# Performance work log

Hardware: AMD Instinct MI355X
Metric: run time of the kernel (lower is better)

Reference implementation:

```python
import jax, jax.numpy as jnp
import numpy as np

N = 50000        # nodes
E = 800000       # edges (before self-loops)
IN = 128         # in_dim
HID = 32         # hidden_dim per head
HEADS = 4
OUT = 64         # out_dim
NEG_SLOPE = 0.2  # PyG GATConv default leaky_relu slope


def setup_inputs() -> dict:
    key = jax.random.key(0)
    ks = jax.random.split(key, 10)
    g = lambda k, shape: jax.random.normal(k, shape, jnp.float32) * 0.1
    x = jax.random.normal(ks[0], (N, IN), jnp.float32)
    edge_index = jax.random.randint(ks[1], (2, E), 0, N, dtype=jnp.int64)
    W1 = g(ks[2], (IN, HEADS * HID))
    att_src1 = g(ks[3], (HEADS, HID))
    att_dst1 = g(ks[4], (HEADS, HID))
    b1 = jnp.zeros((HEADS * HID,), jnp.float32)
    W2 = g(ks[5], (HEADS * HID, OUT))
    att_src2 = g(ks[6], (1, OUT))
    att_dst2 = g(ks[7], (1, OUT))
    b2 = jnp.zeros((OUT,), jnp.float32)
    return {"x": x, "edge_index": edge_index,
            "W1": W1, "att_src1": att_src1, "att_dst1": att_dst1, "b1": b1,
            "W2": W2, "att_src2": att_src2, "att_dst2": att_dst2, "b2": b2}


def gat_layer(x, src, dst, W, a_src, a_dst, b, concat):
    """One PyG-style GATConv layer (self-loops already in src/dst)."""
    H, C = a_src.shape
    h = (x @ W).reshape(-1, H, C)                       # [N, H, C]
    al_s = jnp.sum(h * a_src, axis=-1)                  # [N, H]
    al_d = jnp.sum(h * a_dst, axis=-1)                  # [N, H]
    e = jax.nn.leaky_relu(al_s[src] + al_d[dst], NEG_SLOPE)  # [E', H]
    # segment softmax over incoming edges of each destination node
    m = jax.ops.segment_max(e, dst, num_segments=N)
    m = jnp.where(jnp.isfinite(m), m, 0.0)
    ex = jnp.exp(e - m[dst])
    denom = jax.ops.segment_sum(ex, dst, num_segments=N)
    alpha = ex / (denom[dst] + 1e-16)                   # [E', H]
    out = jax.ops.segment_sum(alpha[:, :, None] * h[src], dst, num_segments=N)  # [N,H,C]
    out = out.reshape(-1, H * C) if concat else out.mean(axis=1)
    return out + b


def reference(x, edge_index, W1, att_src1, att_dst1, b1, W2, att_src2, att_dst2, b2):
    src, dst = edge_index[0], edge_index[1]
    loop = jnp.arange(N, dtype=src.dtype)               # add_self_loops=True default
    src = jnp.concatenate([src, loop])
    dst = jnp.concatenate([dst, loop])
    h = gat_layer(x, src, dst, W1, att_src1, att_dst1, b1, concat=True)   # [N, HEADS*HID]
    h = jax.nn.elu(h)
    return gat_layer(h, src, dst, W2, att_src2, att_dst2, b2, concat=False)  # [N, OUT]
```

## Files before the change

kernel.cpp:

```cpp
#include <hip/hip_runtime.h>

#define NN 50000
#define EE 800000
#define NB 196
#define CHUNK 2048
#define NBLK ((EE + CHUNK - 1) / CHUNK)
#define CAP 6144
#define SSTR 6400

typedef unsigned int uint;
typedef unsigned short ushort;
typedef __attribute__((ext_vector_type(8))) short bf16x8;
typedef __attribute__((ext_vector_type(4))) float f32x4;

__device__ __forceinline__ float lrelu(float v){ return v > 0.f ? v : 0.2f*v; }
__device__ __forceinline__ ushort bf16r(float a){
  uint ua = __float_as_uint(a);
  return (ushort)((ua + 0x7FFFu + ((ua >> 16) & 1u)) >> 16);
}
__device__ __forceinline__ uint pack_bf16(float a, float b){
  return (uint)bf16r(a) | ((uint)bf16r(b) << 16);
}
__device__ __forceinline__ float bf_lo(uint u){ return __uint_as_float(u << 16); }
__device__ __forceinline__ float bf_hi(uint u){ return __uint_as_float(u & 0xFFFF0000u); }

__global__ __launch_bounds__(256) void k_zero(int* __restrict__ ecur){
  int t = threadIdx.x;
  if (t < NB) ecur[t] = 0;
}

__global__ __launch_bounds__(256) void k_bucketize(const int* __restrict__ ei,
                                                   int* __restrict__ ecur, uint* __restrict__ ebuf){
  __shared__ int h[NB];
  __shared__ int sc[256];
  __shared__ int gdelta[NB];
  __shared__ uint P[CHUNK];
  __shared__ int  A[CHUNK];
  int t = threadIdx.x;
  if (t < NB) h[t] = 0;
  __syncthreads();
  int base = blockIdx.x * CHUNK;
  int end = base + CHUNK; if (end > EE) end = EE;
  int bc = end - base;
  int be[8]; int re[8]; uint pe[8];
  #pragma unroll
  for (int q = 0; q < 8; ++q){
    int i = base + t + q*256;
    be[q] = -1;
    if (i < end){
      int s_ = ei[i], d_ = ei[EE + i];
      pe[q] = ((uint)d_ << 16) | (uint)s_;
      int bb = d_ >> 8;
      be[q] = bb;
      re[q] = atomicAdd(&h[bb], 1);
    }
  }
  __syncthreads();
  int v = (t < NB) ? h[t] : 0;
  sc[t] = v;
  __syncthreads();
  for (int off = 1; off < 256; off <<= 1){
    int add = (t >= off) ? sc[t-off] : 0;
    __syncthreads();
    sc[t] += add;
    __syncthreads();
  }
  if (t < NB){
    int lofs = sc[t] - v;
    int g = v ? atomicAdd(&ecur[t], v) : 0;
    gdelta[t] = t*CAP + g - lofs;
    h[t] = lofs;
  }
  __syncthreads();
  #pragma unroll
  for (int q = 0; q < 8; ++q) if (be[q] >= 0){
    int j = h[be[q]] + re[q];
    P[j] = pe[q];
    A[j] = gdelta[be[q]] + j;
  }
  __syncthreads();
  for (int j = t; j < bc; j += 256) ebuf[A[j]] = P[j];
}

__global__ __launch_bounds__(256) void k_csr(const int* __restrict__ ecur,
                                             const uint* __restrict__ ebuf,
                                             int* __restrict__ rptr, int* __restrict__ rend,
                                             ushort* __restrict__ csr){
  __shared__ uint  sbuf[CAP];
  __shared__ ushort rnk[CAP];
  __shared__ int h[256];
  __shared__ int sc[256];
  int b = blockIdx.x, t = threadIdx.x;
  int nd0 = b * 256;
  int ncnt = NN - nd0; if (ncnt > 256) ncnt = 256;
  int cnt = ecur[b]; if (cnt > CAP) cnt = CAP;
  int e0 = b * CAP;
  int cb = b * SSTR;
  h[t] = (t < ncnt) ? 1 : 0;
  for (int j = t; j < cnt; j += 256) sbuf[j] = ebuf[e0 + j];
  __syncthreads();
  for (int j = t; j < cnt; j += 256){
    int local = (sbuf[j] >> 16) & 255;
    rnk[j] = (ushort)atomicAdd(&h[local], 1);
  }
  __syncthreads();
  int v = h[t];
  sc[t] = v;
  __syncthreads();
  for (int off = 1; off < 256; off <<= 1){
    int add = (t >= off) ? sc[t-off] : 0;
    __syncthreads();
    sc[t] += add;
    __syncthreads();
  }
  h[t] = sc[t] - v;
  __syncthreads();
  if (t < ncnt){
    int rs = cb + h[t];
    rptr[nd0 + t] = rs;
    rend[nd0 + t] = rs + v;
    csr[rs] = (ushort)(nd0 + t);
  }
  for (int j = t; j < cnt; j += 256){
    uint p = sbuf[j];
    int local = (p >> 16) & 255;
    csr[cb + h[local] + (int)rnk[j]] = (ushort)(p & 0xFFFFu);
  }
}

__global__ __launch_bounds__(256, 3) void k_gemm1(const float* __restrict__ x, const float* __restrict__ W,
    const float* __restrict__ a_src, const float* __restrict__ a_dst,
    uint* __restrict__ h1b, float* __restrict__ al_s, float* __restrict__ al_d){
  __shared__ ushort Wt[128*136];
  __shared__ ushort Ash[64*136];
  int tid = threadIdx.x;
  int row0 = blockIdx.x * 64;
  const float4* W4 = (const float4*)W;
  #pragma unroll
  for (int f0 = 0; f0 < 4096; f0 += 256){
    int idx4 = f0 + tid;
    int k = idx4 >> 5;
    int n0 = (idx4 & 31) * 4;
    float4 v = W4[idx4];
    Wt[(n0  )*136 + k] = bf16r(v.x);
    Wt[(n0+1)*136 + k] = bf16r(v.y);
    Wt[(n0+2)*136 + k] = bf16r(v.z);
    Wt[(n0+3)*136 + k] = bf16r(v.w);
  }
  const float4* x4 = (const float4*)x;
  #pragma unroll
  for (int f0 = 0; f0 < 2048; f0 += 256){
    int idx4 = f0 + tid;
    int row = idx4 >> 5;
    int q = idx4 & 31;
    float4 v = make_float4(0.f,0.f,0.f,0.f);
    if (row0 + row < NN) v = x4[(size_t)(row0+row)*32 + q];
    *(uint2*)(Ash + row*136 + q*4) = make_uint2(pack_bf16(v.x, v.y), pack_bf16(v.z, v.w));
  }
  __syncthreads();

  int w = tid >> 6, lane = tid & 63;
  int lm = lane & 15, lg = lane >> 4;
  const ushort* Ab = Ash + (w*16 + lm)*136 + lg*8;
  const ushort* Bb = Wt + lm*136 + lg*8;
  f32x4 acc[8];
  #pragma unroll
  for (int i = 0; i < 8; ++i) acc[i] = (f32x4){0.f,0.f,0.f,0.f};
  #pragma unroll
  for (int ks = 0; ks < 4; ++ks){
    bf16x8 af = *(const bf16x8*)(Ab + ks*32);
    #pragma unroll
    for (int ct = 0; ct < 8; ++ct){
      bf16x8 bfr = *(const bf16x8*)(Bb + ct*16*136 + ks*32);
      acc[ct] = __builtin_amdgcn_mfma_f32_16x16x32_bf16(af, bfr, acc[ct], 0, 0, 0);
    }
  }
  int nbase = row0 + w*16 + lg*4;
  float ps[4][4], pd[4][4];
  #pragma unroll
  for (int h = 0; h < 4; ++h)
    #pragma unroll
    for (int r = 0; r < 4; ++r){ ps[h][r] = 0.f; pd[h][r] = 0.f; }
  #pragma unroll
  for (int ct = 0; ct < 8; ++ct){
    int col = ct*16 + lm;
    float ac = a_src[col], dc = a_dst[col];
    #pragma unroll
    for (int r = 0; r < 4; ++r){
      float v = acc[ct][r];
      ps[ct>>1][r] += v*ac;
      pd[ct>>1][r] += v*dc;
      float vp = __shfl_xor(v, 1);
      if ((lm & 1) == 0 && nbase + r < NN)
        h1b[(size_t)(nbase+r)*64 + ct*8 + (lm>>1)] = pack_bf16(v, vp);
    }
  }
  #pragma unroll
  for (int h = 0; h < 4; ++h)
    #pragma unroll
    for (int r = 0; r < 4; ++r){
      float s = ps[h][r], d = pd[h][r];
      s += __shfl_xor(s,1); s += __shfl_xor(s,2); s += __shfl_xor(s,4); s += __shfl_xor(s,8);
      d += __shfl_xor(d,1); d += __shfl_xor(d,2); d += __shfl_xor(d,4); d += __shfl_xor(d,8);
      if (lm == 0 && nbase + r < NN){
        al_s[(nbase+r)*4 + h] = s;
        al_d[(nbase+r)*4 + h] = d;
      }
    }
}

__global__ __launch_bounds__(256) void k_agg1(const int* __restrict__ rptr, const int* __restrict__ rend,
    const ushort* __restrict__ csr,
    const uint* __restrict__ h1b, const float* __restrict__ al_s, const float* __restrict__ al_d,
    const float* __restrict__ b1, uint* __restrict__ h2b){
  int wid  = (blockIdx.x*256 + threadIdx.x) >> 6;
  int lane = threadIdx.x & 63;
  if (wid >= NN) return;
  int half = lane >> 5;
  int li   = lane & 31;
  int h    = li >> 3;
  float ad = al_d[(uint)(wid*4 + h)];
  int rs = rptr[wid];
  int deg = rend[wid] - rs;
  uint rowoff = (uint)(li*2);
  float a0 = 0.f, a1 = 0.f, a2 = 0.f, a3 = 0.f, den = 0.f;
  for (int b0 = 0; b0 < deg; b0 += 64){
    int nb = deg - b0; if (nb > 64) nb = 64;
    int sv = (lane < nb) ? (int)csr[(uint)(rs + b0 + lane)] : 0;
    int jj = 0;
    for (; jj + 8 <= nb; jj += 8){
      int j = jj + half;
      int s0 = __shfl(sv, j), s1 = __shfl(sv, j+2), s2 = __shfl(sv, j+4), s3 = __shfl(sv, j+6);
      float e0 = al_s[(uint)(s0*4 + h)];
      float e1 = al_s[(uint)(s1*4 + h)];
      float e2 = al_s[(uint)(s2*4 + h)];
      float e3 = al_s[(uint)(s3*4 + h)];
      uint2 u0 = *(const uint2*)(h1b + (((uint)s0) << 6) + rowoff);
      uint2 u1 = *(const uint2*)(h1b + (((uint)s1) << 6) + rowoff);
      uint2 u2 = *(const uint2*)(h1b + (((uint)s2) << 6) + rowoff);
      uint2 u3 = *(const uint2*)(h1b + (((uint)s3) << 6) + rowoff);
      float x0 = __expf(lrelu(e0 + ad));
      float x1 = __expf(lrelu(e1 + ad));
      float x2 = __expf(lrelu(e2 + ad));
      float x3 = __expf(lrelu(e3 + ad));
      den += x0 + x1 + x2 + x3;
      a0 += x0*bf_lo(u0.x) + x1*bf_lo(u1.x) + x2*bf_lo(u2.x) + x3*bf_lo(u3.x);
      a1 += x0*bf_hi(u0.x) + x1*bf_hi(u1.x) + x2*bf_hi(u2.x) + x3*bf_hi(u3.x);
      a2 += x0*bf_lo(u0.y) + x1*bf_lo(u1.y) + x2*bf_lo(u2.y) + x3*bf_lo(u3.y);
      a3 += x0*bf_hi(u0.y) + x1*bf_hi(u1.y) + x2*bf_hi(u2.y) + x3*bf_hi(u3.y);
    }
    for (; jj < nb; jj += 2){
      int j = jj + half;
      bool ok = j < nb;
      int s0 = __shfl(sv, ok ? j : 0);
      float e = al_s[(uint)(s0*4 + h)];
      uint2 u = *(const uint2*)(h1b + (((uint)s0) << 6) + rowoff);
      float ex = ok ? __expf(lrelu(e + ad)) : 0.f;
      den += ex;
      a0 += ex*bf_lo(u.x); a1 += ex*bf_hi(u.x);
      a2 += ex*bf_lo(u.y); a3 += ex*bf_hi(u.y);
    }
  }
  den += __shfl_xor(den, 32);
  a0  += __shfl_xor(a0, 32);
  a1  += __shfl_xor(a1, 32);
  a2  += __shfl_xor(a2, 32);
  a3  += __shfl_xor(a3, 32);
  if (half == 0){
    float inv = 1.f/(den + 1e-16f);
    float4 bb = *(const float4*)(b1 + li*4);
    float o0 = a0*inv + bb.x, o1 = a1*inv + bb.y, o2 = a2*inv + bb.z, o3 = a3*inv + bb.w;
    o0 = o0 > 0.f ? o0 : (__expf(o0) - 1.f);
    o1 = o1 > 0.f ? o1 : (__expf(o1) - 1.f);
    o2 = o2 > 0.f ? o2 : (__expf(o2) - 1.f);
    o3 = o3 > 0.f ? o3 : (__expf(o3) - 1.f);
    *(uint2*)(h2b + (size_t)wid*64 + li*2) = make_uint2(pack_bf16(o0,o1), pack_bf16(o2,o3));
  }
}

__global__ __launch_bounds__(256, 4) void k_gemm2(const uint* __restrict__ h2b, const float* __restrict__ W,
    const float* __restrict__ a_src, const float* __restrict__ a_dst,
    uint* __restrict__ gb, float* __restrict__ al_s, float* __restrict__ al_d){
  __shared__ ushort Wt[64*136];
  __shared__ ushort Ash[64*136];
  int tid = threadIdx.x;
  int row0 = blockIdx.x * 64;
  const float4* W4 = (const float4*)W;
  #pragma unroll
  for (int f0 = 0; f0 < 2048; f0 += 256){
    int idx4 = f0 + tid;
    int k = idx4 >> 4;
    int n0 = (idx4 & 15) * 4;
    float4 v = W4[idx4];
    Wt[(n0  )*136 + k] = bf16r(v.x);
    Wt[(n0+1)*136 + k] = bf16r(v.y);
    Wt[(n0+2)*136 + k] = bf16r(v.z);
    Wt[(n0+3)*136 + k] = bf16r(v.w);
  }
  #pragma unroll
  for (int f0 = 0; f0 < 4096; f0 += 256){
    int idx = f0 + tid;
    int row = idx >> 6;
    int q = idx & 63;
    uint u = 0;
    if (row0 + row < NN) u = h2b[(size_t)(row0+row)*64 + q];
    *(uint*)(Ash + row*136 + q*2) = u;
  }
  __syncthreads();

  int w = tid >> 6, lane = tid & 63;
  int lm = lane & 15, lg = lane >> 4;
  const ushort* Ab = Ash + (w*16 + lm)*136 + lg*8;
  const ushort* Bb = Wt + lm*136 + lg*8;
  f32x4 acc[4];
  #pragma unroll
  for (int i = 0; i < 4; ++i) acc[i] = (f32x4){0.f,0.f,0.f,0.f};
  #pragma unroll
  for (int ks = 0; ks < 4; ++ks){
    bf16x8 af = *(const bf16x8*)(Ab + ks*32);
    #pragma unroll
    for (int ct = 0; ct < 4; ++ct){
      bf16x8 bfr = *(const bf16x8*)(Bb + ct*16*136 + ks*32);
      acc[ct] = __builtin_amdgcn_mfma_f32_16x16x32_bf16(af, bfr, acc[ct], 0, 0, 0);
    }
  }
  int nbase = row0 + w*16 + lg*4;
  float ps[4], pd[4];
  #pragma unroll
  for (int r = 0; r < 4; ++r){ ps[r] = 0.f; pd[r] = 0.f; }
  #pragma unroll
  for (int ct = 0; ct < 4; ++ct){
    int col = ct*16 + lm;
    float ac = a_src[col], dc = a_dst[col];
    #pragma unroll
    for (int r = 0; r < 4; ++r){
      float v = acc[ct][r];
      ps[r] += v*ac;
      pd[r] += v*dc;
      float vp = __shfl_xor(v, 1);
      if ((lm & 1) == 0 && nbase + r < NN)
        gb[(size_t)(nbase+r)*32 + ct*8 + (lm>>1)] = pack_bf16(v, vp);
    }
  }
  #pragma unroll
  for (int r = 0; r < 4; ++r){
    float s = ps[r], d = pd[r];
    s += __shfl_xor(s,1); s += __shfl_xor(s,2); s += __shfl_xor(s,4); s += __shfl_xor(s,8);
    d += __shfl_xor(d,1); d += __shfl_xor(d,2); d += __shfl_xor(d,4); d += __shfl_xor(d,8);
    if (lm == 0 && nbase + r < NN){
      al_s[nbase+r] = s;
      al_d[nbase+r] = d;
    }
  }
}

__global__ __launch_bounds__(256) void k_agg2(const int* __restrict__ rptr, const int* __restrict__ rend,
    const ushort* __restrict__ csr,
    const uint* __restrict__ gb, const float* __restrict__ al_s, const float* __restrict__ al_d,
    const float* __restrict__ b2, float* __restrict__ out){
  int wid  = (blockIdx.x*256 + threadIdx.x) >> 6;
  int lane = threadIdx.x & 63;
  if (wid >= NN) return;
  int half = lane >> 5;
  int li   = lane & 31;
  float ad = al_d[(uint)wid];
  int rs = rptr[wid];
  int deg = rend[wid] - rs;
  float a0 = 0.f, a1 = 0.f, den = 0.f;
  for (int b0 = 0; b0 < deg; b0 += 64){
    int nb = deg - b0; if (nb > 64) nb = 64;
    int sv = (lane < nb) ? (int)csr[(uint)(rs + b0 + lane)] : 0;
    int jj = 0;
    for (; jj + 8 <= nb; jj += 8){
      int j = jj + half;
      int s0 = __shfl(sv, j), s1 = __shfl(sv, j+2), s2 = __shfl(sv, j+4), s3 = __shfl(sv, j+6);
      float e0 = al_s[(uint)s0];
      float e1 = al_s[(uint)s1];
      float e2 = al_s[(uint)s2];
      float e3 = al_s[(uint)s3];
      uint u0 = gb[(((uint)s0) << 5) + (uint)li];
      uint u1 = gb[(((uint)s1) << 5) + (uint)li];
      uint u2 = gb[(((uint)s2) << 5) + (uint)li];
      uint u3 = gb[(((uint)s3) << 5) + (uint)li];
      float x0 = __expf(lrelu(e0 + ad));
      float x1 = __expf(lrelu(e1 + ad));
      float x2 = __expf(lrelu(e2 + ad));
      float x3 = __expf(lrelu(e3 + ad));
      den += x0 + x1 + x2 + x3;
      a0 += x0*bf_lo(u0) + x1*bf_lo(u1) + x2*bf_lo(u2) + x3*bf_lo(u3);
      a1 += x0*bf_hi(u0) + x1*bf_hi(u1) + x2*bf_hi(u2) + x3*bf_hi(u3);
    }
    for (; jj < nb; jj += 2){
      int j = jj + half;
      bool ok = j < nb;
      int s0 = __shfl(sv, ok ? j : 0);
      float e = al_s[(uint)s0];
      uint u = gb[(((uint)s0) << 5) + (uint)li];
      float ex = ok ? __expf(lrelu(e + ad)) : 0.f;
      den += ex;
      a0 += ex*bf_lo(u); a1 += ex*bf_hi(u);
    }
  }
  den += __shfl_xor(den, 32);
  a0  += __shfl_xor(a0, 32);
  a1  += __shfl_xor(a1, 32);
  if (half == 0){
    float inv = 1.f/(den + 1e-16f);
    float2 bb = *(const float2*)(b2 + li*2);
    *(float2*)(out + (size_t)wid*64 + li*2) = make_float2(a0*inv + bb.x, a1*inv + bb.y);
  }
}

extern "C" void kernel_launch(void* const* d_in, const int* in_sizes, int n_in,
                              void* d_out, int out_size, void* d_ws, size_t ws_size,
                              hipStream_t stream){
  const float* x   = (const float*)d_in[0];
  const int*   ei  = (const int*)d_in[1];
  const float* W1  = (const float*)d_in[2];
  const float* as1 = (const float*)d_in[3];
  const float* ad1 = (const float*)d_in[4];
  const float* b1  = (const float*)d_in[5];
  const float* W2  = (const float*)d_in[6];
  const float* as2 = (const float*)d_in[7];
  const float* ad2 = (const float*)d_in[8];
  const float* b2  = (const float*)d_in[9];
  float* out = (float*)d_out;
  (void)in_sizes; (void)n_in; (void)out_size; (void)ws_size;

  char* p = (char*)d_ws;
  size_t off = 0;
  auto alloc = [&](size_t bytes)->char*{
    char* r = p + off; off += (bytes + 255) & ~size_t(255); return r;
  };
  uint*  h1b   = (uint*)alloc((size_t)NN*64*4);
  uint*  h2b   = (uint*)alloc((size_t)NN*64*4);
  uint*  gb    = (uint*)alloc((size_t)NN*32*4);
  float* al1s  = (float*)alloc((size_t)NN*4*4);
  float* al1d  = (float*)alloc((size_t)NN*4*4);
  float* al2s  = (float*)alloc((size_t)NN*4);
  float* al2d  = (float*)alloc((size_t)NN*4);
  int*   rptr  = (int*)alloc((size_t)NN*4);
  int*   rend  = (int*)alloc((size_t)NN*4);
  ushort* csr  = (ushort*)alloc((size_t)NB*SSTR*2);
  uint*  ebuf  = (uint*)alloc((size_t)NB*CAP*4);
  int*   ecur  = (int*)alloc((size_t)NB*4);

  k_zero<<<1, 256, 0, stream>>>(ecur);
  k_bucketize<<<NBLK, 256, 0, stream>>>(ei, ecur, ebuf);
  k_csr<<<NB, 256, 0, stream>>>(ecur, ebuf, rptr, rend, csr);
  k_gemm1<<<(NN+63)/64, 256, 0, stream>>>(x, W1, as1, ad1, h1b, al1s, al1d);
  k_agg1<<<(NN*64+255)/256, 256, 0, stream>>>(rptr, rend, csr, h1b, al1s, al1d, b1, h2b);
  k_gemm2<<<(NN+63)/64, 256, 0, stream>>>(h2b, W2, as2, ad2, gb, al2s, al2d);
  k_agg2<<<(NN*64+255)/256, 256, 0, stream>>>(rptr, rend, csr, gb, al2s, al2d, b2, out);
}
```

Measured before the change: 137.1 us.

## Fuse bucketize with gemm1 and layer-1 aggregation with gemm2

Merges edge bucketizing and the layer-1 GEMM into one launch whose blocks split by block index, sharing shared memory through a union. Layer-1 aggregation is fused with the layer-2 GEMM: each 512-thread block aggregates 64 nodes into shared memory and then runs MFMA on them, which removes the h2b round trip through global memory. The zero kernel is replaced by a memset, and there are fewer launches overall. In exchange, the fused aggregation blocks are larger and heavier on registers and shared memory, which may lower occupancy and load balance for the gather phase.

```diff
diff --git a/kernel.cpp b/kernel.cpp
--- a/kernel.cpp
+++ b/kernel.cpp
@@ -5,6 +5,7 @@
 #define NB 196
 #define CHUNK 2048
 #define NBLK ((EE + CHUNK - 1) / CHUNK)
+#define GB1 ((NN + 63) / 64)
 #define CAP 6144
 #define SSTR 6400
 
@@ -24,62 +25,137 @@
 __device__ __forceinline__ float bf_lo(uint u){ return __uint_as_float(u << 16); }
 __device__ __forceinline__ float bf_hi(uint u){ return __uint_as_float(u & 0xFFFF0000u); }
 
-__global__ __launch_bounds__(256) void k_zero(int* __restrict__ ecur){
+union BG1Shared {
+  struct { int h[NB]; int sc[256]; int gdelta[NB]; uint P[CHUNK]; int A[CHUNK]; } bk;
+  struct { ushort Wt[128*136]; ushort Ash[64*136]; } gm;
+};
+
+__global__ __launch_bounds__(256, 3) void k_bg1(const int* __restrict__ ei,
+    int* __restrict__ ecur, uint* __restrict__ ebuf,
+    const float* __restrict__ x, const float* __restrict__ W,
+    const float* __restrict__ a_src, const float* __restrict__ a_dst,
+    uint* __restrict__ h1b, float* __restrict__ al_s, float* __restrict__ al_d){
+  __shared__ BG1Shared S;
   int t = threadIdx.x;
-  if (t < NB) ecur[t] = 0;
-}
-
-__global__ __launch_bounds__(256) void k_bucketize(const int* __restrict__ ei,
-                                                   int* __restrict__ ecur, uint* __restrict__ ebuf){
-  __shared__ int h[NB];
-  __shared__ int sc[256];
-  __shared__ int gdelta[NB];
-  __shared__ uint P[CHUNK];
-  __shared__ int  A[CHUNK];
-  int t = threadIdx.x;
-  if (t < NB) h[t] = 0;
-  __syncthreads();
-  int base = blockIdx.x * CHUNK;
-  int end = base + CHUNK; if (end > EE) end = EE;
-  int bc = end - base;
-  int be[8]; int re[8]; uint pe[8];
-  #pragma unroll
-  for (int q = 0; q < 8; ++q){
-    int i = base + t + q*256;
-    be[q] = -1;
-    if (i < end){
-      int s_ = ei[i], d_ = ei[EE + i];
-      pe[q] = ((uint)d_ << 16) | (uint)s_;
-      int bb = d_ >> 8;
-      be[q] = bb;
-      re[q] = atomicAdd(&h[bb], 1);
-    }
-  }
-  __syncthreads();
-  int v = (t < NB) ? h[t] : 0;
-  sc[t] = v;
-  __syncthreads();
-  for (int off = 1; off < 256; off <<= 1){
-    int add = (t >= off) ? sc[t-off] : 0;
-    __syncthreads();
-    sc[t] += add;
-    __syncthreads();
-  }
-  if (t < NB){
-    int lofs = sc[t] - v;
-    int g = v ? atomicAdd(&ecur[t], v) : 0;
-    gdelta[t] = t*CAP + g - lofs;
-    h[t] = lofs;
-  }
-  __syncthreads();
-  #pragma unroll
-  for (int q = 0; q < 8; ++q) if (be[q] >= 0){
-    int j = h[be[q]] + re[q];
-    P[j] = pe[q];
-    A[j] = gdelta[be[q]] + j;
-  }
-  __syncthreads();
-  for (int j = t; j < bc; j += 256) ebuf[A[j]] = P[j];
+  if (blockIdx.x < NBLK){
+    if (t < NB) S.bk.h[t] = 0;
+    __syncthreads();
+    int base = blockIdx.x * CHUNK;
+    int end = base + CHUNK; if (end > EE) end = EE;
+    int bc = end - base;
+    int be[8]; int re[8]; uint pe[8];
+    #pragma unroll
+    for (int q = 0; q < 8; ++q){
+      int i = base + t + q*256;
+      be[q] = -1;
+      if (i < end){
+        int s_ = ei[i], d_ = ei[EE + i];
+        pe[q] = ((uint)d_ << 16) | (uint)s_;
+        int bb = d_ >> 8;
+        be[q] = bb;
+        re[q] = atomicAdd(&S.bk.h[bb], 1);
+      }
+    }
+    __syncthreads();
+    int v = (t < NB) ? S.bk.h[t] : 0;
+    S.bk.sc[t] = v;
+    __syncthreads();
+    for (int off = 1; off < 256; off <<= 1){
+      int add = (t >= off) ? S.bk.sc[t-off] : 0;
+      __syncthreads();
+      S.bk.sc[t] += add;
+      __syncthreads();
+    }
+    if (t < NB){
+      int lofs = S.bk.sc[t] - v;
+      int g = v ? atomicAdd(&ecur[t], v) : 0;
+      S.bk.gdelta[t] = t*CAP + g - lofs;
+      S.bk.h[t] = lofs;
+    }
+    __syncthreads();
+    #pragma unroll
+    for (int q = 0; q < 8; ++q) if (be[q] >= 0){
+      int j = S.bk.h[be[q]] + re[q];
+      S.bk.P[j] = pe[q];
+      S.bk.A[j] = S.bk.gdelta[be[q]] + j;
+    }
+    __syncthreads();
+    for (int j = t; j < bc; j += 256) ebuf[S.bk.A[j]] = S.bk.P[j];
+    return;
+  }
+  int row0 = (blockIdx.x - NBLK) * 64;
+  const float4* W4 = (const float4*)W;
+  #pragma unroll
+  for (int f0 = 0; f0 < 4096; f0 += 256){
+    int idx4 = f0 + t;
+    int k = idx4 >> 5;
+    int n0 = (idx4 & 31) * 4;
+    float4 v = W4[idx4];
+    S.gm.Wt[(n0  )*136 + k] = bf16r(v.x);
+    S.gm.Wt[(n0+1)*136 + k] = bf16r(v.y);
+    S.gm.Wt[(n0+2)*136 + k] = bf16r(v.z);
+    S.gm.Wt[(n0+3)*136 + k] = bf16r(v.w);
+  }
+  const float4* x4 = (const float4*)x;
+  #pragma unroll
+  for (int f0 = 0; f0 < 2048; f0 += 256){
+    int idx4 = f0 + t;
+    int row = idx4 >> 5;
+    int q = idx4 & 31;
+    float4 v = make_float4(0.f,0.f,0.f,0.f);
+    if (row0 + row < NN) v = x4[(size_t)(row0+row)*32 + q];
+    *(uint2*)(S.gm.Ash + row*136 + q*4) = make_uint2(pack_bf16(v.x, v.y), pack_bf16(v.z, v.w));
+  }
+  __syncthreads();
+
+  int w = t >> 6, lane = t & 63;
+  int lm = lane & 15, lg = lane >> 4;
+  const ushort* Ab = S.gm.Ash + (w*16 + lm)*136 + lg*8;
+  const ushort* Bb = S.gm.Wt + lm*136 + lg*8;
+  f32x4 acc[8];
+  #pragma unroll
+  for (int i = 0; i < 8; ++i) acc[i] = (f32x4){0.f,0.f,0.f,0.f};
+  #pragma unroll
+  for (int ks = 0; ks < 4; ++ks){
+    bf16x8 af = *(const bf16x8*)(Ab + ks*32);
+    #pragma unroll
+    for (int ct = 0; ct < 8; ++ct){
+      bf16x8 bfr = *(const bf16x8*)(Bb + ct*16*136 + ks*32);
+      acc[ct] = __builtin_amdgcn_mfma_f32_16x16x32_bf16(af, bfr, acc[ct], 0, 0, 0);
+    }
+  }
+  int nbase = row0 + w*16 + lg*4;
+  float ps[4][4], pd[4][4];
+  #pragma unroll
+  for (int h = 0; h < 4; ++h)
+    #pragma unroll
+    for (int r = 0; r < 4; ++r){ ps[h][r] = 0.f; pd[h][r] = 0.f; }
+  #pragma unroll
+  for (int ct = 0; ct < 8; ++ct){
+    int col = ct*16 + lm;
+    float ac = a_src[col], dc = a_dst[col];
+    #pragma unroll
+    for (int r = 0; r < 4; ++r){
+      float v = acc[ct][r];
+      ps[ct>>1][r] += v*ac;
+      pd[ct>>1][r] += v*dc;
+      float vp = __shfl_xor(v, 1);
+      if ((lm & 1) == 0 && nbase + r < NN)
+        h1b[(size_t)(nbase+r)*64 + ct*8 + (lm>>1)] = pack_bf16(v, vp);
+    }
+  }
+  #pragma unroll
+  for (int h = 0; h < 4; ++h)
+    #pragma unroll
+    for (int r = 0; r < 4; ++r){
+      float s = ps[h][r], d = pd[h][r];
+      s += __shfl_xor(s,1); s += __shfl_xor(s,2); s += __shfl_xor(s,4); s += __shfl_xor(s,8);
+      d += __shfl_xor(d,1); d += __shfl_xor(d,2); d += __shfl_xor(d,4); d += __shfl_xor(d,8);
+      if (lm == 0 && nbase + r < NN){
+        al_s[(nbase+r)*4 + h] = s;
+        al_d[(nbase+r)*4 + h] = d;
+      }
+    }
 }
 
 __global__ __launch_bounds__(256) void k_csr(const int* __restrict__ ecur,
@@ -128,166 +204,21 @@
   }
 }
 
-__global__ __launch_bounds__(256, 3) void k_gemm1(const float* __restrict__ x, const float* __restrict__ W,
-    const float* __restrict__ a_src, const float* __restrict__ a_dst,
-    uint* __restrict__ h1b, float* __restrict__ al_s, float* __restrict__ al_d){
-  __shared__ ushort Wt[128*136];
-  __shared__ ushort Ash[64*136];
-  int tid = threadIdx.x;
-  int row0 = blockIdx.x * 64;
-  const float4* W4 = (const float4*)W;
-  #pragma unroll
-  for (int f0 = 0; f0 < 4096; f0 += 256){
-    int idx4 = f0 + tid;
-    int k = idx4 >> 5;
-    int n0 = (idx4 & 31) * 4;
-    float4 v = W4[idx4];
-    Wt[(n0  )*136 + k] = bf16r(v.x);
-    Wt[(n0+1)*136 + k] = bf16r(v.y);
-    Wt[(n0+2)*136 + k] = bf16r(v.z);
-    Wt[(n0+3)*136 + k] = bf16r(v.w);
-  }
-  const float4* x4 = (const float4*)x;
-  #pragma unroll
-  for (int f0 = 0; f0 < 2048; f0 += 256){
-    int idx4 = f0 + tid;
-    int row = idx4 >> 5;
-    int q = idx4 & 31;
-    float4 v = make_float4(0.f,0.f,0.f,0.f);
-    if (row0 + row < NN) v = x4[(size_t)(row0+row)*32 + q];
-    *(uint2*)(Ash + row*136 + q*4) = make_uint2(pack_bf16(v.x, v.y), pack_bf16(v.z, v.w));
-  }
-  __syncthreads();
-
-  int w = tid >> 6, lane = tid & 63;
-  int lm = lane & 15, lg = lane >> 4;
-  const ushort* Ab = Ash + (w*16 + lm)*136 + lg*8;
-  const ushort* Bb = Wt + lm*136 + lg*8;
-  f32x4 acc[8];
-  #pragma unroll
-  for (int i = 0; i < 8; ++i) acc[i] = (f32x4){0.f,0.f,0.f,0.f};
-  #pragma unroll
-  for (int ks = 0; ks < 4; ++ks){
-    bf16x8 af = *(const bf16x8*)(Ab + ks*32);
-    #pragma unroll
-    for (int ct = 0; ct < 8; ++ct){
-      bf16x8 bfr = *(const bf16x8*)(Bb + ct*16*136 + ks*32);
-      acc[ct] = __builtin_amdgcn_mfma_f32_16x16x32_bf16(af, bfr, acc[ct], 0, 0, 0);
-    }
-  }
-  int nbase = row0 + w*16 + lg*4;
-  float ps[4][4], pd[4][4];
-  #pragma unroll
-  for (int h = 0; h < 4; ++h)
-    #pragma unroll
-    for (int r = 0; r < 4; ++r){ ps[h][r] = 0.f; pd[h][r] = 0.f; }
-  #pragma unroll
-  for (int ct = 0; ct < 8; ++ct){
-    int col = ct*16 + lm;
-    float ac = a_src[col], dc = a_dst[col];
-    #pragma unroll
-    for (int r = 0; r < 4; ++r){
-      float v = acc[ct][r];
-      ps[ct>>1][r] += v*ac;
-      pd[ct>>1][r] += v*dc;
-      float vp = __shfl_xor(v, 1);
-      if ((lm & 1) == 0 && nbase + r < NN)
-        h1b[(size_t)(nbase+r)*64 + ct*8 + (lm>>1)] = pack_bf16(v, vp);
-    }
-  }
-  #pragma unroll
-  for (int h = 0; h < 4; ++h)
-    #pragma unroll
-    for (int r = 0; r < 4; ++r){
-      float s = ps[h][r], d = pd[h][r];
-      s += __shfl_xor(s,1); s += __shfl_xor(s,2); s += __shfl_xor(s,4); s += __shfl_xor(s,8);
-      d += __shfl_xor(d,1); d += __shfl_xor(d,2); d += __shfl_xor(d,4); d += __shfl_xor(d,8);
-      if (lm == 0 && nbase + r < NN){
-        al_s[(nbase+r)*4 + h] = s;
-        al_d[(nbase+r)*4 + h] = d;
-      }
-    }
-}
-
-__global__ __launch_bounds__(256) void k_agg1(const int* __restrict__ rptr, const int* __restrict__ rend,
+__global__ __launch_bounds__(512, 2) void k_ag12(const int* __restrict__ rptr, const int* __restrict__ rend,
     const ushort* __restrict__ csr,
-    const uint* __restrict__ h1b, const float* __restrict__ al_s, const float* __restrict__ al_d,
-    const float* __restrict__ b1, uint* __restrict__ h2b){
-  int wid  = (blockIdx.x*256 + threadIdx.x) >> 6;
-  int lane = threadIdx.x & 63;
-  if (wid >= NN) return;
-  int half = lane >> 5;
-  int li   = lane & 31;
-  int h    = li >> 3;
-  float ad = al_d[(uint)(wid*4 + h)];
-  int rs = rptr[wid];
-  int deg = rend[wid] - rs;
-  uint rowoff = (uint)(li*2);
-  float a0 = 0.f, a1 = 0.f, a2 = 0.f, a3 = 0.f, den = 0.f;
-  for (int b0 = 0; b0 < deg; b0 += 64){
-    int nb = deg - b0; if (nb > 64) nb = 64;
-    int sv = (lane < nb) ? (int)csr[(uint)(rs + b0 + lane)] : 0;
-    int jj = 0;
-    for (; jj + 8 <= nb; jj += 8){
-      int j = jj + half;
-      int s0 = __shfl(sv, j), s1 = __shfl(sv, j+2), s2 = __shfl(sv, j+4), s3 = __shfl(sv, j+6);
-      float e0 = al_s[(uint)(s0*4 + h)];
-      float e1 = al_s[(uint)(s1*4 + h)];
-      float e2 = al_s[(uint)(s2*4 + h)];
-      float e3 = al_s[(uint)(s3*4 + h)];
-      uint2 u0 = *(const uint2*)(h1b + (((uint)s0) << 6) + rowoff);
-      uint2 u1 = *(const uint2*)(h1b + (((uint)s1) << 6) + rowoff);
-      uint2 u2 = *(const uint2*)(h1b + (((uint)s2) << 6) + rowoff);
-      uint2 u3 = *(const uint2*)(h1b + (((uint)s3) << 6) + rowoff);
-      float x0 = __expf(lrelu(e0 + ad));
-      float x1 = __expf(lrelu(e1 + ad));
-      float x2 = __expf(lrelu(e2 + ad));
-      float x3 = __expf(lrelu(e3 + ad));
-      den += x0 + x1 + x2 + x3;
-      a0 += x0*bf_lo(u0.x) + x1*bf_lo(u1.x) + x2*bf_lo(u2.x) + x3*bf_lo(u3.x);
-      a1 += x0*bf_hi(u0.x) + x1*bf_hi(u1.x) + x2*bf_hi(u2.x) + x3*bf_hi(u3.x);
-      a2 += x0*bf_lo(u0.y) + x1*bf_lo(u1.y) + x2*bf_lo(u2.y) + x3*bf_lo(u3.y);
-      a3 += x0*bf_hi(u0.y) + x1*bf_hi(u1.y) + x2*bf_hi(u2.y) + x3*bf_hi(u3.y);
-    }
-    for (; jj < nb; jj += 2){
-      int j = jj + half;
-      bool ok = j < nb;
-      int s0 = __shfl(sv, ok ? j : 0);
-      float e = al_s[(uint)(s0*4 + h)];
-      uint2 u = *(const uint2*)(h1b + (((uint)s0) << 6) + rowoff);
-      float ex = ok ? __expf(lrelu(e + ad)) : 0.f;
-      den += ex;
-      a0 += ex*bf_lo(u.x); a1 += ex*bf_hi(u.x);
-      a2 += ex*bf_lo(u.y); a3 += ex*bf_hi(u.y);
-    }
-  }
-  den += __shfl_xor(den, 32);
-  a0  += __shfl_xor(a0, 32);
-  a1  += __shfl_xor(a1, 32);
-  a2  += __shfl_xor(a2, 32);
-  a3  += __shfl_xor(a3, 32);
-  if (half == 0){
-    float inv = 1.f/(den + 1e-16f);
-    float4 bb = *(const float4*)(b1 + li*4);
-    float o0 = a0*inv + bb.x, o1 = a1*inv + bb.y, o2 = a2*inv + bb.z, o3 = a3*inv + bb.w;
-    o0 = o0 > 0.f ? o0 : (__expf(o0) - 1.f);
-    o1 = o1 > 0.f ? o1 : (__expf(o1) - 1.f);
-    o2 = o2 > 0.f ? o2 : (__expf(o2) - 1.f);
-    o3 = o3 > 0.f ? o3 : (__expf(o3) - 1.f);
-    *(uint2*)(h2b + (size_t)wid*64 + li*2) = make_uint2(pack_bf16(o0,o1), pack_bf16(o2,o3));
-  }
-}
-
-__global__ __launch_bounds__(256, 4) void k_gemm2(const uint* __restrict__ h2b, const float* __restrict__ W,
-    const float* __restrict__ a_src, const float* __restrict__ a_dst,
-    uint* __restrict__ gb, float* __restrict__ al_s, float* __restrict__ al_d){
+    const uint* __restrict__ h1b, const float* __restrict__ al1s, const float* __restrict__ al1d,
+    const float* __restrict__ b1, const float* __restrict__ W2,
+    const float* __restrict__ a2s, const float* __restrict__ a2d,
+    uint* __restrict__ gb, float* __restrict__ al2s, float* __restrict__ al2d){
   __shared__ ushort Wt[64*136];
   __shared__ ushort Ash[64*136];
+  __shared__ float ssum[64], dsum[64];
   int tid = threadIdx.x;
-  int row0 = blockIdx.x * 64;
-  const float4* W4 = (const float4*)W;
-  #pragma unroll
-  for (int f0 = 0; f0 < 2048; f0 += 256){
+  int nd0 = blockIdx.x * 64;
+  if (tid < 64){ ssum[tid] = 0.f; dsum[tid] = 0.f; }
+  const float4* W4 = (const float4*)W2;
+  #pragma unroll
+  for (int f0 = 0; f0 < 2048; f0 += 512){
     int idx4 = f0 + tid;
     int k = idx4 >> 4;
     int n0 = (idx4 & 15) * 4;
@@ -297,41 +228,98 @@
     Wt[(n0+2)*136 + k] = bf16r(v.z);
     Wt[(n0+3)*136 + k] = bf16r(v.w);
   }
-  #pragma unroll
-  for (int f0 = 0; f0 < 4096; f0 += 256){
-    int idx = f0 + tid;
-    int row = idx >> 6;
-    int q = idx & 63;
-    uint u = 0;
-    if (row0 + row < NN) u = h2b[(size_t)(row0+row)*64 + q];
-    *(uint*)(Ash + row*136 + q*2) = u;
-  }
-  __syncthreads();
-
   int w = tid >> 6, lane = tid & 63;
+  int half = lane >> 5;
+  int li   = lane & 31;
+  int h    = li >> 3;
+  uint rowoff = (uint)(li*2);
+  uint* AshU = (uint*)Ash;
+  for (int i = 0; i < 8; ++i){
+    int nloc = w*8 + i;
+    int wid = nd0 + nloc;
+    if (wid >= NN) break;
+    float ad = al1d[(uint)(wid*4 + h)];
+    int rs = rptr[wid];
+    int deg = rend[wid] - rs;
+    float a0 = 0.f, a1 = 0.f, a2 = 0.f, a3 = 0.f, den = 0.f;
+    for (int b0 = 0; b0 < deg; b0 += 64){
+      int nb = deg - b0; if (nb > 64) nb = 64;
+      int sv = (lane < nb) ? (int)csr[(uint)(rs + b0 + lane)] : 0;
+      int jj = 0;
+      for (; jj + 8 <= nb; jj += 8){
+        int j = jj + half;
+        int s0 = __shfl(sv, j), s1 = __shfl(sv, j+2), s2 = __shfl(sv, j+4), s3 = __shfl(sv, j+6);
+        float e0 = al1s[(uint)(s0*4 + h)];
+        float e1 = al1s[(uint)(s1*4 + h)];
+        float e2 = al1s[(uint)(s2*4 + h)];
+        float e3 = al1s[(uint)(s3*4 + h)];
+        uint2 u0 = *(const uint2*)(h1b + (((uint)s0) << 6) + rowoff);
+        uint2 u1 = *(const uint2*)(h1b + (((uint)s1) << 6) + rowoff);
+        uint2 u2 = *(const uint2*)(h1b + (((uint)s2) << 6) + rowoff);
+        uint2 u3 = *(const uint2*)(h1b + (((uint)s3) << 6) + rowoff);
+        float x0 = __expf(lrelu(e0 + ad));
+        float x1 = __expf(lrelu(e1 + ad));
+        float x2 = __expf(lrelu(e2 + ad));
+        float x3 = __expf(lrelu(e3 + ad));
+        den += x0 + x1 + x2 + x3;
+        a0 += x0*bf_lo(u0.x) + x1*bf_lo(u1.x) + x2*bf_lo(u2.x) + x3*bf_lo(u3.x);
+        a1 += x0*bf_hi(u0.x) + x1*bf_hi(u1.x) + x2*bf_hi(u2.x) + x3*bf_hi(u3.x);
+        a2 += x0*bf_lo(u0.y) + x1*bf_lo(u1.y) + x2*bf_lo(u2.y) + x3*bf_lo(u3.y);
+        a3 += x0*bf_hi(u0.y) + x1*bf_hi(u1.y) + x2*bf_hi(u2.y) + x3*bf_hi(u3.y);
+      }
+      for (; jj < nb; jj += 2){
+        int j = jj + half;
+        bool ok = j < nb;
+        int s0 = __shfl(sv, ok ? j : 0);
+        float e = al1s[(uint)(s0*4 + h)];
+        uint2 u = *(const uint2*)(h1b + (((uint)s0) << 6) + rowoff);
+        float ex = ok ? __expf(lrelu(e + ad)) : 0.f;
+        den += ex;
+        a0 += ex*bf_lo(u.x); a1 += ex*bf_hi(u.x);
+        a2 += ex*bf_lo(u.y); a3 += ex*bf_hi(u.y);
+      }
+    }
+    den += __shfl_xor(den, 32);
+    a0  += __shfl_xor(a0, 32);
+    a1  += __shfl_xor(a1, 32);
+    a2  += __shfl_xor(a2, 32);
+    a3  += __shfl_xor(a3, 32);
+    if (half == 0){
+      float inv = 1.f/(den + 1e-16f);
+      float4 bb = *(const float4*)(b1 + li*4);
+      float o0 = a0*inv + bb.x, o1 = a1*inv + bb.y, o2 = a2*inv + bb.z, o3 = a3*inv + bb.w;
+      o0 = o0 > 0.f ? o0 : (__expf(o0) - 1.f);
+      o1 = o1 > 0.f ? o1 : (__expf(o1) - 1.f);
+      o2 = o2 > 0.f ? o2 : (__expf(o2) - 1.f);
+      o3 = o3 > 0.f ? o3 : (__expf(o3) - 1.f);
+      *(uint2*)(AshU + nloc*68 + li*2) = make_uint2(pack_bf16(o0,o1), pack_bf16(o2,o3));
+    }
+  }
+  __syncthreads();
   int lm = lane & 15, lg = lane >> 4;
-  const ushort* Ab = Ash + (w*16 + lm)*136 + lg*8;
-  const ushort* Bb = Wt + lm*136 + lg*8;
-  f32x4 acc[4];
-  #pragma unroll
-  for (int i = 0; i < 4; ++i) acc[i] = (f32x4){0.f,0.f,0.f,0.f};
+  int rw = w & 3, cw = w >> 2;
+  const ushort* Ab = Ash + (rw*16 + lm)*136 + lg*8;
+  const ushort* Bb = Wt + (cw*32 + lm)*136 + lg*8;
+  f32x4 acc[2];
+  acc[0] = (f32x4){0.f,0.f,0.f,0.f};
+  acc[1] = (f32x4){0.f,0.f,0.f,0.f};
   #pragma unroll
   for (int ks = 0; ks < 4; ++ks){
     bf16x8 af = *(const bf16x8*)(Ab + ks*32);
     #pragma unroll
-    for (int ct = 0; ct < 4; ++ct){
+    for (int ct = 0; ct < 2; ++ct){
       bf16x8 bfr = *(const bf16x8*)(Bb + ct*16*136 + ks*32);
       acc[ct] = __builtin_amdgcn_mfma_f32_16x16x32_bf16(af, bfr, acc[ct], 0, 0, 0);
     }
   }
-  int nbase = row0 + w*16 + lg*4;
+  int nbase = nd0 + rw*16 + lg*4;
   float ps[4], pd[4];
   #pragma unroll
   for (int r = 0; r < 4; ++r){ ps[r] = 0.f; pd[r] = 0.f; }
   #pragma unroll
-  for (int ct = 0; ct < 4; ++ct){
-    int col = ct*16 + lm;
-    float ac = a_src[col], dc = a_dst[col];
+  for (int ct = 0; ct < 2; ++ct){
+    int col = cw*32 + ct*16 + lm;
+    float ac = a2s[col], dc = a2d[col];
     #pragma unroll
     for (int r = 0; r < 4; ++r){
       float v = acc[ct][r];
@@ -339,7 +327,7 @@
       pd[r] += v*dc;
       float vp = __shfl_xor(v, 1);
       if ((lm & 1) == 0 && nbase + r < NN)
-        gb[(size_t)(nbase+r)*32 + ct*8 + (lm>>1)] = pack_bf16(v, vp);
+        gb[(size_t)(nbase+r)*32 + cw*16 + ct*8 + (lm>>1)] = pack_bf16(v, vp);
     }
   }
   #pragma unroll
@@ -347,10 +335,16 @@
     float s = ps[r], d = pd[r];
     s += __shfl_xor(s,1); s += __shfl_xor(s,2); s += __shfl_xor(s,4); s += __shfl_xor(s,8);
     d += __shfl_xor(d,1); d += __shfl_xor(d,2); d += __shfl_xor(d,4); d += __shfl_xor(d,8);
-    if (lm == 0 && nbase + r < NN){
-      al_s[nbase+r] = s;
-      al_d[nbase+r] = d;
-    }
+    if (lm == 0){
+      int nloc = rw*16 + lg*4 + r;
+      atomicAdd(&ssum[nloc], s);
+      atomicAdd(&dsum[nloc], d);
+    }
+  }
+  __syncthreads();
+  if (tid < 64 && nd0 + tid < NN){
+    al2s[nd0 + tid] = ssum[tid];
+    al2d[nd0 + tid] = dsum[tid];
   }
 }
 
@@ -433,7 +427,6 @@
     char* r = p + off; off += (bytes + 255) & ~size_t(255); return r;
   };
   uint*  h1b   = (uint*)alloc((size_t)NN*64*4);
-  uint*  h2b   = (uint*)alloc((size_t)NN*64*4);
   uint*  gb    = (uint*)alloc((size_t)NN*32*4);
   float* al1s  = (float*)alloc((size_t)NN*4*4);
   float* al1d  = (float*)alloc((size_t)NN*4*4);
@@ -445,11 +438,9 @@
   uint*  ebuf  = (uint*)alloc((size_t)NB*CAP*4);
   int*   ecur  = (int*)alloc((size_t)NB*4);
 
-  k_zero<<<1, 256, 0, stream>>>(ecur);
-  k_bucketize<<<NBLK, 256, 0, stream>>>(ei, ecur, ebuf);
+  hipMemsetAsync(ecur, 0, (size_t)NB*4, stream);
+  k_bg1<<<NBLK + GB1, 256, 0, stream>>>(ei, ecur, ebuf, x, W1, as1, ad1, h1b, al1s, al1d);
   k_csr<<<NB, 256, 0, stream>>>(ecur, ebuf, rptr, rend, csr);
-  k_gemm1<<<(NN+63)/64, 256, 0, stream>>>(x, W1, as1, ad1, h1b, al1s, al1d);
-  k_agg1<<<(NN*64+255)/256, 256, 0, stream>>>(rptr, rend, csr, h1b, al1s, al1d, b1, h2b);
-  k_gemm2<<<(NN+63)/64, 256, 0, stream>>>(h2b, W2, as2, ad2, gb, al2s, al2d);
+  k_ag12<<<GB1, 512, 0, stream>>>(rptr, rend, csr, h1b, al1s, al1d, b1, W2, as2, ad2, gb, al2s, al2d);
   k_agg2<<<(NN*64+255)/256, 256, 0, stream>>>(rptr, rend, csr, gb, al2s, al2d, b2, out);
 }
```

Result: faster. 129.0 us (-5.9%).
